# Kernel optimization log

Measured on AMD Instinct MI355X. Metric: run time of the kernel, lower is better.

Reference implementation:

```python
import jax, jax.numpy as jnp
import numpy as np

E = 8
HIDDEN = 1024
INTER = 4096
CAPS = np.array([512, 1024, 2048, 4096, 1024, 512, 2048, 1024], dtype=np.int64)  # sum = 12288
TOTAL = int(CAPS.sum())


def setup_inputs() -> dict:
    key = jax.random.key(0)
    k1, k2, k3, k4, k5 = jax.random.split(key, 5)
    s1 = 1.0 / np.sqrt(HIDDEN)
    s2 = 1.0 / np.sqrt(INTER)
    return {
        "inter_state": jax.random.normal(k1, (TOTAL, HIDDEN), dtype=jnp.float32),
        "w1": jax.random.normal(k2, (E, INTER, HIDDEN), dtype=jnp.float32) * s1,
        "b1": jax.random.normal(k3, (E, INTER), dtype=jnp.float32) * s1,
        "w2": jax.random.normal(k4, (E, HIDDEN, INTER), dtype=jnp.float32) * s2,
        "b2": jax.random.normal(k5, (E, HIDDEN), dtype=jnp.float32) * s2,
        "capacities": jnp.asarray(CAPS),
    }


def reference(inter_state, w1, b1, w2, b2, capacities):
    # Grouped GEMM: tokens are contiguous per expert with sizes = capacities.
    # Capacities are routing metadata (static for slicing).
    caps = np.asarray(capacities)
    offs = np.concatenate([[0], np.cumsum(caps)]).astype(np.int64)
    outs = []
    for e in range(caps.shape[0]):  # small fixed expert loop
        x = inter_state[int(offs[e]):int(offs[e + 1])]      # [cap_e, hidden]
        h = x @ w1[e].T + b1[e]                              # [cap_e, inter]
        outs.append(h @ w2[e].T + b2[e])                     # [cap_e, hidden]
    return jnp.concatenate(outs, axis=0)                     # [total, hidden]
```

## Files before the change

### kernel.cpp

```cpp
#include <hip/hip_runtime.h>
#include <hip/hip_bf16.h>

#define DEV __device__ __forceinline__

typedef __bf16 bf16x8 __attribute__((ext_vector_type(8)));
typedef float  f32x4  __attribute__((ext_vector_type(4)));


DEV unsigned short f2bf(float f) {
  union { float f; unsigned u; } v; v.f = f;
  unsigned u = v.u;
  return (unsigned short)((u + 0x7FFFu + ((u >> 16) & 1u)) >> 16);
}

DEV void gld_lds16(const void* g, void* l) {
  __builtin_amdgcn_global_load_lds(
      (const __attribute__((address_space(1))) unsigned int*)g,
      (__attribute__((address_space(3))) unsigned int*)l, 16, 0, 0);
}

template <int K_, int N_, bool OUT_BF16, bool HAS_BIAS, int EDIV>
__global__ __launch_bounds__(512, 2)
void gemm8(const unsigned short* __restrict__ A,
           const unsigned short* __restrict__ B,
           const float* __restrict__ bias, void* __restrict__ Cv) {
  __shared__ __align__(128) char lds[3][49152];

  const int t    = threadIdx.x;
  const int lane = t & 63;
  const int wv   = t >> 6;
  const int wm   = wv >> 1;
  const int wn   = wv & 1;
  const int fr   = lane & 15;
  const int fq   = lane >> 4;

  constexpr int NCT = N_ / 128;
  constexpr int NT  = K_ / 64;

  int bid = blockIdx.x;
  const int nwg = gridDim.x;
  bid = (bid & 7) * (nwg >> 3) + (bid >> 3);

  const int rt = bid / NCT;
  const int ct = bid - rt * NCT;

  int e;
  if constexpr (EDIV > 0) {
    e = rt / EDIV;
  } else {
    const int cums[9] = {0, 2, 6, 14, 30, 34, 36, 44, 48};
    e = 0;
#pragma unroll
    for (int i = 1; i < 8; ++i) e += (rt >= cums[i]) ? 1 : 0;
  }

  const int grow0 = rt * 256;
  const int nloc0 = ct * 128;
  const unsigned short* Bg = B + (size_t)e * N_ * K_;

  f32x4 acc[4][4];
#pragma unroll
  for (int i = 0; i < 4; ++i)
#pragma unroll
    for (int j = 0; j < 4; ++j) acc[i][j] = (f32x4){0.f, 0.f, 0.f, 0.f};

  auto stage = [&](int buf, int tk) {
    const int kb = tk * 64;
    char* Abase = lds[buf];
    char* Bbase = lds[buf] + 32768;
#pragma unroll
    for (int s = 0; s < 4; ++s) {
      int o  = s * 8192 + wv * 1024 + lane * 16;
      int r  = o >> 7;
      int cb = (o & 127) ^ ((r & 7) << 4);
      gld_lds16(A + (size_t)(grow0 + r) * K_ + kb + (cb >> 1),
                Abase + s * 8192 + wv * 1024);
    }
#pragma unroll
    for (int s = 0; s < 2; ++s) {
      int o  = s * 8192 + wv * 1024 + lane * 16;
      int r  = o >> 7;
      int cb = (o & 127) ^ ((r & 7) << 4);
      gld_lds16(Bg + (size_t)(nloc0 + r) * K_ + kb + (cb >> 1),
                Bbase + s * 8192 + wv * 1024);
    }
  };

  auto compute = [&](int buf) {
    char* Abase = lds[buf];
    char* Bbase = lds[buf] + 32768;
    bf16x8 af[4][2], bf[4][2];
#pragma unroll
    for (int mi = 0; mi < 4; ++mi) {
      int r = wm * 64 + mi * 16 + fr;
#pragma unroll
      for (int k = 0; k < 2; ++k) {
        int cb = (k * 64 + fq * 16) ^ ((r & 7) << 4);
        af[mi][k] = *(bf16x8*)(Abase + r * 128 + cb);
      }
    }
#pragma unroll
    for (int ni = 0; ni < 4; ++ni) {
      int r = wn * 64 + ni * 16 + fr;
#pragma unroll
      for (int k = 0; k < 2; ++k) {
        int cb = (k * 64 + fq * 16) ^ ((r & 7) << 4);
        bf[ni][k] = *(bf16x8*)(Bbase + r * 128 + cb);
      }
    }
    __builtin_amdgcn_s_setprio(1);
#pragma unroll
    for (int k = 0; k < 2; ++k)
#pragma unroll
      for (int mi = 0; mi < 4; ++mi)
#pragma unroll
        for (int ni = 0; ni < 4; ++ni)
          acc[mi][ni] = __builtin_amdgcn_mfma_f32_16x16x32_bf16(
              af[mi][k], bf[ni][k], acc[mi][ni], 0, 0, 0);
    __builtin_amdgcn_s_setprio(0);
  };

  stage(0, 0);
  stage(1, 1);
  int cur = 0;
  for (int tk = 0; tk < NT; ++tk) {
    if (tk + 2 < NT) {
      int nb = cur + 2; if (nb >= 3) nb -= 3;
      stage(nb, tk + 2);
      asm volatile("s_waitcnt vmcnt(12)" ::: "memory");
    } else if (tk + 1 < NT) {
      asm volatile("s_waitcnt vmcnt(6)" ::: "memory");
    } else {
      asm volatile("s_waitcnt vmcnt(0)" ::: "memory");
    }
    __builtin_amdgcn_s_barrier();
    __builtin_amdgcn_sched_barrier(0);
    compute(cur);
    __builtin_amdgcn_sched_barrier(0);
    asm volatile("s_waitcnt lgkmcnt(0)" ::: "memory");
    __builtin_amdgcn_sched_barrier(0);
    __builtin_amdgcn_s_barrier();
    ++cur; if (cur >= 3) cur = 0;
  }

#pragma unroll
  for (int ni = 0; ni < 4; ++ni) {
    int nloc = nloc0 + wn * 64 + ni * 16 + fr;
    float bv = 0.f;
    if constexpr (HAS_BIAS) bv = (bias + (size_t)e * N_)[nloc];
#pragma unroll
    for (int mi = 0; mi < 4; ++mi) {
      int m = grow0 + wm * 64 + mi * 16 + fq * 4;
#pragma unroll
      for (int j = 0; j < 4; ++j) {
        float val = acc[mi][ni][j] + bv;
        if constexpr (OUT_BF16)
          ((unsigned short*)Cv)[(size_t)(m + j) * N_ + nloc] = f2bf(val);
        else
          ((float*)Cv)[(size_t)(m + j) * N_ + nloc] = val;
      }
    }
  }
}

DEV int swz(int r, int cbyte) {
  return (r * 64 + cbyte) ^ (((r >> 1) & 7) << 4);
}

template <int K_, int N_, int NCT_, int AMODE, int BMODE, bool OUT_BF16,
          bool HAS_BIAS, int EDIV>
__global__ __launch_bounds__(256)
void gemm_expert(const void* __restrict__ Av, const void* __restrict__ Bv,
                 const float* __restrict__ bias, void* __restrict__ Cv) {
  __shared__ char lds[2][12288];

  const int t    = threadIdx.x;
  const int lane = t & 63;
  const int wv   = t >> 6;
  const int wr   = wv >> 1;
  const int wc   = wv & 1;
  const int fr   = lane & 15;
  const int fq   = lane >> 4;

  int bid = blockIdx.x;
  const int nwg = gridDim.x;
  if ((nwg & 7) == 0) bid = (bid & 7) * (nwg >> 3) + (bid >> 3);

  const int rt = bid / NCT_;
  const int ct = bid - rt * NCT_;

  int e;
  if constexpr (EDIV > 0) {
    e = rt / EDIV;
  } else {
    const int cums[9] = {0, 4, 12, 28, 60, 68, 72, 88, 96};
    e = 0;
#pragma unroll
    for (int i = 1; i < 8; ++i) e += (rt >= cums[i]) ? 1 : 0;
  }

  const int grow0 = rt * 128;
  const int nloc0 = ct * 64;

  f32x4 acc[4][2];
#pragma unroll
  for (int i = 0; i < 4; ++i)
#pragma unroll
    for (int j = 0; j < 2; ++j) acc[i][j] = (f32x4){0.f, 0.f, 0.f, 0.f};

  const unsigned short* Ab = (const unsigned short*)Av;
  const float*          Af = (const float*)Av;
  const unsigned short* Bb = (const unsigned short*)Bv + (size_t)e * N_ * K_;
  const float*          Bf = (const float*)Bv + (size_t)e * N_ * K_;

  auto stage = [&](int buf, int kb) {
    char* As = lds[buf];
    char* Bs = lds[buf] + 8192;
    if constexpr (AMODE == 1) {
#pragma unroll
      for (int s = 0; s < 2; ++s) {
        int o = (wv * 2 + s) * 1024 + lane * 16;
        int p = o ^ (((o >> 7) & 7) << 4);
        gld_lds16(Ab + (size_t)(grow0 + (p >> 6)) * K_ + kb + ((p & 63) >> 1),
                  As + (wv * 2 + s) * 1024);
      }
    } else {
#pragma unroll
      for (int it = 0; it < 4; ++it) {
        int q = t + it * 256, r = q >> 3, c = (q & 7) * 4;
        float4 f = *(const float4*)(Af + (size_t)(grow0 + r) * K_ + kb + c);
        ushort4 v = {f2bf(f.x), f2bf(f.y), f2bf(f.z), f2bf(f.w)};
        *(ushort4*)(As + swz(r, c * 2)) = v;
      }
    }
    if constexpr (BMODE == 1) {
      int o = wv * 1024 + lane * 16;
      int p = o ^ (((o >> 7) & 7) << 4);
      gld_lds16(Bb + (size_t)(nloc0 + (p >> 6)) * K_ + kb + ((p & 63) >> 1),
                Bs + wv * 1024);
    } else {
#pragma unroll
      for (int it = 0; it < 2; ++it) {
        int q = t + it * 256, r = q >> 3, c = (q & 7) * 4;
        float4 f = *(const float4*)(Bf + (size_t)(nloc0 + r) * K_ + kb + c);
        ushort4 v = {f2bf(f.x), f2bf(f.y), f2bf(f.z), f2bf(f.w)};
        *(ushort4*)(Bs + swz(r, c * 2)) = v;
      }
    }
  };

  auto compute = [&](int buf) {
    char* As = lds[buf];
    char* Bs = lds[buf] + 8192;
    bf16x8 af[4], bfg[2];
#pragma unroll
    for (int mi = 0; mi < 4; ++mi)
      af[mi] = *(bf16x8*)(As + swz(wr * 64 + mi * 16 + fr, fq * 16));
#pragma unroll
    for (int ni = 0; ni < 2; ++ni)
      bfg[ni] = *(bf16x8*)(Bs + swz(wc * 32 + ni * 16 + fr, fq * 16));
#pragma unroll
    for (int mi = 0; mi < 4; ++mi)
#pragma unroll
      for (int ni = 0; ni < 2; ++ni)
        acc[mi][ni] = __builtin_amdgcn_mfma_f32_16x16x32_bf16(
            af[mi], bfg[ni], acc[mi][ni], 0, 0, 0);
  };

  int cur = 0;
  stage(0, 0);
  __syncthreads();
#pragma unroll 2
  for (int kb = 32; kb < K_; kb += 32) {
    stage(cur ^ 1, kb);
    compute(cur);
    __syncthreads();
    cur ^= 1;
  }
  compute(cur);

#pragma unroll
  for (int ni = 0; ni < 2; ++ni) {
    int nloc = nloc0 + wc * 32 + ni * 16 + fr;
    float bv = 0.f;
    if constexpr (HAS_BIAS) bv = (bias + (size_t)e * N_)[nloc];
#pragma unroll
    for (int mi = 0; mi < 4; ++mi) {
      int m = grow0 + wr * 64 + mi * 16 + fq * 4;
#pragma unroll
      for (int j = 0; j < 4; ++j) {
        float val = acc[mi][ni][j] + bv;
        if constexpr (OUT_BF16)
          ((unsigned short*)Cv)[(size_t)(m + j) * N_ + nloc] = f2bf(val);
        else
          ((float*)Cv)[(size_t)(m + j) * N_ + nloc] = val;
      }
    }
  }
}

__global__ __launch_bounds__(256)
void transpose_w1(const float* __restrict__ w1, unsigned short* __restrict__ w1t) {
  __shared__ unsigned short tl[64 * 68];
  int b = blockIdx.x;
  int jt = b & 15, kt = (b >> 4) & 63, e = b >> 10;
  const float* src = w1 + ((size_t)e * 4096 + kt * 64) * 1024 + jt * 64;
  int t = threadIdx.x;
#pragma unroll
  for (int it = 0; it < 4; ++it) {
    int q = t + it * 256, kr = q >> 4, jc = (q & 15) * 4;
    float4 f = *(const float4*)(src + (size_t)kr * 1024 + jc);
    ushort4 v = {f2bf(f.x), f2bf(f.y), f2bf(f.z), f2bf(f.w)};
    *(ushort4*)&tl[kr * 68 + jc] = v;
  }
  __syncthreads();
  unsigned short* dst = w1t + ((size_t)e * 1024 + jt * 64) * 4096 + kt * 64;
#pragma unroll
  for (int it = 0; it < 4; ++it) {
    int q = t + it * 256, jr = q >> 4, kc = (q & 15) * 4;
    ushort4 v = {tl[(kc + 0) * 68 + jr], tl[(kc + 1) * 68 + jr],
                 tl[(kc + 2) * 68 + jr], tl[(kc + 3) * 68 + jr]};
    *(ushort4*)(dst + (size_t)jr * 4096 + kc) = v;
  }
}

template <bool STORE_BF>
__global__ __launch_bounds__(256)
void conv_w2_bias(const float* __restrict__ w2, const float* __restrict__ b1,
                  const float* __restrict__ b2, unsigned short* __restrict__ w2bf,
                  float* __restrict__ bc) {
  int row = blockIdx.x, e = row >> 10, t = threadIdx.x;
  const float* src = w2 + (size_t)row * 4096;
  const float* b1e = b1 + (size_t)e * 4096;
  float acc = 0.f;
#pragma unroll
  for (int it = 0; it < 4; ++it) {
    int c = (t + it * 256) * 4;
    float4 f = *(const float4*)(src + c);
    float4 g = *(const float4*)(b1e + c);
    acc += f.x * g.x + f.y * g.y + f.z * g.z + f.w * g.w;
    if constexpr (STORE_BF) {
      ushort4 v = {f2bf(f.x), f2bf(f.y), f2bf(f.z), f2bf(f.w)};
      *(ushort4*)(w2bf + (size_t)row * 4096 + c) = v;
    }
  }
#pragma unroll
  for (int o = 32; o > 0; o >>= 1) acc += __shfl_down(acc, o);
  __shared__ float red[4];
  if ((t & 63) == 0) red[t >> 6] = acc;
  __syncthreads();
  if (t == 0) bc[row] = red[0] + red[1] + red[2] + red[3] + b2[row];
}

__global__ __launch_bounds__(256)
void conv_f32_bf16(const float* __restrict__ in, unsigned short* __restrict__ out,
                   int n4) {
  for (int i = blockIdx.x * 256 + threadIdx.x; i < n4; i += gridDim.x * 256) {
    float4 f = *(const float4*)(in + (size_t)i * 4);
    ushort4 v = {f2bf(f.x), f2bf(f.y), f2bf(f.z), f2bf(f.w)};
    *(ushort4*)(out + (size_t)i * 4) = v;
  }
}

extern "C" void kernel_launch(void* const* d_in, const int* in_sizes, int n_in,
                              void* d_out, int out_size, void* d_ws, size_t ws_size,
                              hipStream_t stream) {
  const float* x  = (const float*)d_in[0];
  const float* w1 = (const float*)d_in[1];
  const float* b1 = (const float*)d_in[2];
  const float* w2 = (const float*)d_in[3];
  const float* b2 = (const float*)d_in[4];

  char* ws = (char*)d_ws;
  unsigned short* w1t = (unsigned short*)ws;
  const size_t NEED_T2 = 151126016, NEED_T3 = 176291840;

  if (ws_size >= NEED_T2) {
    unsigned short* w2bf = (unsigned short*)(ws + 67108864);
    unsigned short* Wc   = (unsigned short*)(ws + 134217728);
    float*          bc   = (float*)(ws + 150994944);

    transpose_w1<<<8192, 256, 0, stream>>>(w1, w1t);
    conv_w2_bias<true><<<8192, 256, 0, stream>>>(w2, b1, b2, w2bf, bc);
    gemm8<4096, 1024, true, false, 4>
        <<<256, 512, 0, stream>>>(w2bf, w1t, nullptr, Wc);
    if (ws_size >= NEED_T3) {
      unsigned short* xbf = (unsigned short*)(ws + 151126016);
      conv_f32_bf16<<<2048, 256, 0, stream>>>(x, xbf, 12288 * 1024 / 4);
      gemm8<1024, 1024, false, true, 0>
          <<<384, 512, 0, stream>>>(xbf, Wc, bc, (float*)d_out);
    } else {
      gemm_expert<1024, 1024, 16, 0, 1, false, true, 0>
          <<<1536, 256, 0, stream>>>(x, Wc, bc, d_out);
    }
  } else {
    unsigned short* Wc = (unsigned short*)(ws + 67108864);
    float*          bc = (float*)(ws + 83886080);

    transpose_w1<<<8192, 256, 0, stream>>>(w1, w1t);
    conv_w2_bias<false><<<8192, 256, 0, stream>>>(w2, b1, b2, nullptr, bc);
    gemm_expert<4096, 1024, 16, 0, 1, true, false, 8>
        <<<1024, 256, 0, stream>>>(w2, w1t, nullptr, Wc);
    gemm_expert<1024, 1024, 16, 0, 1, false, true, 0>
        <<<1536, 256, 0, stream>>>(x, Wc, bc, d_out);
  }
}
```

Baseline: 204.7 us.

## Switch to double-buffered LDS and split fragment loads to overlap with MFMA

Cuts the LDS ring from three to two 48KB stages, so only one K tile is prefetched ahead instead of two. Inside each tile, the A-fragment reads are split in two halves, and the MFMAs on the first half start after a partial lgkmcnt wait while the second half is still loading. This frees 48KB of LDS per block and hides LDS read latency behind MFMA. In exchange the global-load prefetch depth is shallower, which may expose more memory latency.

```diff
diff --git a/kernel.cpp b/kernel.cpp
--- a/kernel.cpp
+++ b/kernel.cpp
@@ -18,13 +18,18 @@
       (const __attribute__((address_space(1))) unsigned int*)g,
       (__attribute__((address_space(3))) unsigned int*)l, 16, 0, 0);
 }
+
+#define WAITVM(N) asm volatile("s_waitcnt vmcnt(" #N ")" ::: "memory"); \
+                  __builtin_amdgcn_sched_barrier(0)
+#define WAITLG(N) asm volatile("s_waitcnt lgkmcnt(" #N ")" ::: "memory"); \
+                  __builtin_amdgcn_sched_barrier(0)
 
 template <int K_, int N_, bool OUT_BF16, bool HAS_BIAS, int EDIV>
 __global__ __launch_bounds__(512, 2)
 void gemm8(const unsigned short* __restrict__ A,
            const unsigned short* __restrict__ B,
            const float* __restrict__ bias, void* __restrict__ Cv) {
-  __shared__ __align__(128) char lds[3][49152];
+  __shared__ __align__(128) char lds[2][49152];
 
   const int t    = threadIdx.x;
   const int lane = t & 63;
@@ -86,61 +91,65 @@
     }
   };
 
-  auto compute = [&](int buf) {
-    char* Abase = lds[buf];
-    char* Bbase = lds[buf] + 32768;
+  stage(0, 0);
+  for (int tk = 0; tk < NT; ++tk) {
+    const int cur = tk & 1;
+    if (tk + 1 < NT) {
+      stage(cur ^ 1, tk + 1);
+      WAITVM(6);
+    } else {
+      WAITVM(0);
+    }
+    __builtin_amdgcn_s_barrier();
+
+    char* Abase = lds[cur];
+    char* Bbase = lds[cur] + 32768;
     bf16x8 af[4][2], bf[4][2];
 #pragma unroll
-    for (int mi = 0; mi < 4; ++mi) {
+    for (int mi = 0; mi < 2; ++mi) {
       int r = wm * 64 + mi * 16 + fr;
 #pragma unroll
-      for (int k = 0; k < 2; ++k) {
-        int cb = (k * 64 + fq * 16) ^ ((r & 7) << 4);
-        af[mi][k] = *(bf16x8*)(Abase + r * 128 + cb);
-      }
+      for (int k = 0; k < 2; ++k)
+        af[mi][k] = *(bf16x8*)(Abase + r * 128 + ((k * 64 + fq * 16) ^ ((r & 7) << 4)));
     }
 #pragma unroll
     for (int ni = 0; ni < 4; ++ni) {
       int r = wn * 64 + ni * 16 + fr;
 #pragma unroll
-      for (int k = 0; k < 2; ++k) {
-        int cb = (k * 64 + fq * 16) ^ ((r & 7) << 4);
-        bf[ni][k] = *(bf16x8*)(Bbase + r * 128 + cb);
-      }
-    }
+      for (int k = 0; k < 2; ++k)
+        bf[ni][k] = *(bf16x8*)(Bbase + r * 128 + ((k * 64 + fq * 16) ^ ((r & 7) << 4)));
+    }
+    __builtin_amdgcn_sched_barrier(0);
+#pragma unroll
+    for (int mi = 2; mi < 4; ++mi) {
+      int r = wm * 64 + mi * 16 + fr;
+#pragma unroll
+      for (int k = 0; k < 2; ++k)
+        af[mi][k] = *(bf16x8*)(Abase + r * 128 + ((k * 64 + fq * 16) ^ ((r & 7) << 4)));
+    }
+    WAITLG(4);
     __builtin_amdgcn_s_setprio(1);
 #pragma unroll
     for (int k = 0; k < 2; ++k)
 #pragma unroll
-      for (int mi = 0; mi < 4; ++mi)
+      for (int mi = 0; mi < 2; ++mi)
 #pragma unroll
         for (int ni = 0; ni < 4; ++ni)
           acc[mi][ni] = __builtin_amdgcn_mfma_f32_16x16x32_bf16(
               af[mi][k], bf[ni][k], acc[mi][ni], 0, 0, 0);
     __builtin_amdgcn_s_setprio(0);
-  };
-
-  stage(0, 0);
-  stage(1, 1);
-  int cur = 0;
-  for (int tk = 0; tk < NT; ++tk) {
-    if (tk + 2 < NT) {
-      int nb = cur + 2; if (nb >= 3) nb -= 3;
-      stage(nb, tk + 2);
-      asm volatile("s_waitcnt vmcnt(12)" ::: "memory");
-    } else if (tk + 1 < NT) {
-      asm volatile("s_waitcnt vmcnt(6)" ::: "memory");
-    } else {
-      asm volatile("s_waitcnt vmcnt(0)" ::: "memory");
-    }
+    WAITLG(0);
+    __builtin_amdgcn_s_setprio(1);
+#pragma unroll
+    for (int k = 0; k < 2; ++k)
+#pragma unroll
+      for (int mi = 2; mi < 4; ++mi)
+#pragma unroll
+        for (int ni = 0; ni < 4; ++ni)
+          acc[mi][ni] = __builtin_amdgcn_mfma_f32_16x16x32_bf16(
+              af[mi][k], bf[ni][k], acc[mi][ni], 0, 0, 0);
+    __builtin_amdgcn_s_setprio(0);
     __builtin_amdgcn_s_barrier();
-    __builtin_amdgcn_sched_barrier(0);
-    compute(cur);
-    __builtin_amdgcn_sched_barrier(0);
-    asm volatile("s_waitcnt lgkmcnt(0)" ::: "memory");
-    __builtin_amdgcn_sched_barrier(0);
-    __builtin_amdgcn_s_barrier();
-    ++cur; if (cur >= 3) cur = 0;
   }
 
 #pragma unroll
```

Measured after the change: 204.2 us. About the same (-0.2%).
